# Kernel tuning notes

Hardware: AMD Instinct MI355X
Metric: run time of the kernel (lower is better)

## Reference

```python
import jax, jax.numpy as jnp
import numpy as np

N_SPIKES = 16384
N_UNITS = 256
N_NEIGHB = 128
RANK = 5
NC = 64
NC_OBS = 12
N_CAND = 10  # n_candidates*(n_search+1)+n_explore = 3*3+1
D = RANK * NC_OBS
LOG2PI = 1.8378770664093453


def setup_inputs() -> dict:
    key = jax.random.key(0)
    ks = jax.random.split(key, 8)
    features = jax.random.normal(ks[0], (N_SPIKES, RANK, NC_OBS), dtype=jnp.float32)
    mu = jax.random.normal(ks[1], (N_UNITS, RANK, NC), dtype=jnp.float32)
    # PSD inverse marginal covariances per neighborhood: A A^T / D + I
    A = jax.random.normal(ks[2], (N_NEIGHB, D, D), dtype=jnp.float32)
    Coo_inv = jnp.einsum('nij,nkj->nik', A, A) / D + jnp.eye(D, dtype=jnp.float32)
    # logdet of Coo = -logdet(Coo_inv)
    sign, ld = jnp.linalg.slogdet(Coo_inv)
    Coo_logdet = (-ld).astype(jnp.float32)
    log_proportions = jax.nn.log_softmax(jax.random.normal(ks[3], (N_UNITS,), dtype=jnp.float32))
    noise_log_prop = jnp.float32(-3.0)
    cands = jax.random.randint(ks[4], (N_SPIKES, N_CAND), 0, N_UNITS)
    nid = jax.random.randint(ks[5], (N_SPIKES,), 0, N_NEIGHB)
    # distinct observed channels per neighborhood, sorted
    perm = jnp.argsort(jax.random.uniform(ks[6], (N_NEIGHB, NC)), axis=1)
    obs_ix = jnp.sort(perm[:, :NC_OBS], axis=1)
    return {
        'features': features, 'mu': mu, 'Coo_inv': Coo_inv,
        'Coo_logdet': Coo_logdet, 'log_proportions': log_proportions,
        'noise_log_prop': noise_log_prop, 'cands': cands, 'nid': nid,
        'obs_ix': obs_ix,
    }


def reference(features, mu, Coo_inv, Coo_logdet, log_proportions, noise_log_prop, cands, nid, obs_ix):
    N, R, nco = features.shape
    Nu = mu.shape[0]
    C = cands.shape[1]
    Dd = R * nco
    # --- gather per-spike / per-candidate tables (load_batch) ---
    obs = obs_ix[nid]                                   # (N, nco)
    mu_c = mu[cands]                                    # (N, C, R, NC)
    nu = jnp.take_along_axis(mu_c, obs[:, None, None, :], axis=3)  # (N, C, R, nco)
    Cinv = Coo_inv[nid]                                 # (N, D, D)
    base = Coo_logdet[nid] + Dd * LOG2PI                # (N,)
    # --- truncated Gaussian log-likelihoods (te_batch) ---
    xf = features.reshape(N, Dd)
    xc = xf[:, None, :] - nu.reshape(N, C, Dd)          # (N, C, D)
    y = jnp.einsum('nde,nce->ncd', Cinv, xc)
    mahal = jnp.einsum('ncd,ncd->nc', y, xc)
    ll = log_proportions[cands] - 0.5 * (base[:, None] + mahal)
    yn = jnp.einsum('nde,ne->nd', Cinv, xf)
    mahal_noise = jnp.einsum('nd,nd->n', yn, xf)
    ll_noise = noise_log_prop - 0.5 * (base + mahal_noise)
    logliks = jnp.concatenate([ll, ll_noise[:, None]], axis=1)  # (N, C+1)
    Q = jax.nn.softmax(logliks, axis=1)
    # --- scatter-add sufficient statistics per unit ---
    Qc = Q[:, :C]
    seg = cands.reshape(-1)
    counts = jax.ops.segment_sum(Qc.reshape(-1), seg, num_segments=Nu)
    xw = (Qc[:, :, None] * xf[:, None, :]).reshape(N * C, Dd)
    xsum = jax.ops.segment_sum(xw, seg, num_segments=Nu)
    return jnp.concatenate([counts[:, None], xsum], axis=1)  # (Nu, D+1)
```

## Files before the change

### kernel.cpp

```cpp
#include <hip/hip_runtime.h>

#define N_SPIKES 16384
#define N_UNITS  256
#define N_NEIGHB 128
#define RANK     5
#define NC       64
#define NC_OBS   12
#define N_CAND   10
#define DD       60
#define DD4      15
#define OUT_COLS 61
#define OUT_SIZE (N_UNITS * OUT_COLS)
#define NSB      8
#define SCAP     192
#define CNT_PAD  4
#define CAP      (NSB * SCAP)
#define CPAD     64

__global__ __launch_bounds__(256) void precompute_kernel(
    const float* __restrict__ mu, const float* __restrict__ Coo_inv,
    const int* __restrict__ obs_ix, const float* __restrict__ log_prop,
    float* __restrict__ w_buf, float* __restrict__ b_buf,
    int* __restrict__ gcount)
{
    __shared__ float cinv[DD * CPAD];
    __shared__ float nu_lds[64 * 61];
    __shared__ float q2_lds[64 * 4];

    const int b   = blockIdx.x;
    const int h   = b >> 2;
    const int ub  = (b & 3) * 64;
    const int tid = threadIdx.x;

    if (tid < 16) gcount[b * 16 + tid] = 0;

    {
        const float* __restrict__ src = Coo_inv + h * DD * DD;
        for (int idx = tid; idx < DD * CPAD; idx += 256) {
            const int e = idx >> 6;
            const int c = idx & 63;
            cinv[idx] = (c < DD) ? src[e * DD + c] : 0.f;
        }
    }

    {
        const int ut  = tid >> 2;
        const int dqt = tid & 3;
        const float* __restrict__ mub = mu + (ub + ut) * (RANK * NC);
#pragma unroll
        for (int j = 0; j < DD4; ++j) {
            const int d  = dqt * DD4 + j;
            const int r  = d / NC_OBS;
            const int jj = d - r * NC_OBS;
            const int ch = obs_ix[h * NC_OBS + jj];
            nu_lds[ut * 61 + d] = mub[r * NC + ch];
        }
    }
    __syncthreads();

    const int lane = tid & 63;
    const int dq   = __builtin_amdgcn_readfirstlane(tid >> 6);
    const int u    = ub + lane;
    const int p    = h * N_UNITS + u;

    float wreg[16];
#pragma unroll
    for (int j = 0; j < 16; ++j) wreg[j] = 0.f;

    const float* __restrict__ Cslice = cinv + dq * 16;
#pragma unroll 4
    for (int e = 0; e < DD; ++e) {
        const float nu_e = nu_lds[lane * 61 + e];
        const float4* __restrict__ c4 =
            (const float4*)(Cslice + e * CPAD);
        const float4 c0 = c4[0], c1 = c4[1], c2 = c4[2], c3 = c4[3];
        wreg[ 0] = fmaf(c0.x, nu_e, wreg[ 0]);
        wreg[ 1] = fmaf(c0.y, nu_e, wreg[ 1]);
        wreg[ 2] = fmaf(c0.z, nu_e, wreg[ 2]);
        wreg[ 3] = fmaf(c0.w, nu_e, wreg[ 3]);
        wreg[ 4] = fmaf(c1.x, nu_e, wreg[ 4]);
        wreg[ 5] = fmaf(c1.y, nu_e, wreg[ 5]);
        wreg[ 6] = fmaf(c1.z, nu_e, wreg[ 6]);
        wreg[ 7] = fmaf(c1.w, nu_e, wreg[ 7]);
        wreg[ 8] = fmaf(c2.x, nu_e, wreg[ 8]);
        wreg[ 9] = fmaf(c2.y, nu_e, wreg[ 9]);
        wreg[10] = fmaf(c2.z, nu_e, wreg[10]);
        wreg[11] = fmaf(c2.w, nu_e, wreg[11]);
        wreg[12] = fmaf(c3.x, nu_e, wreg[12]);
        wreg[13] = fmaf(c3.y, nu_e, wreg[13]);
        wreg[14] = fmaf(c3.z, nu_e, wreg[14]);
        wreg[15] = fmaf(c3.w, nu_e, wreg[15]);
    }

    float q2 = 0.f;
#pragma unroll
    for (int j = 0; j < 16; ++j) {
        const int c = dq * 16 + j;
        const float nv = nu_lds[lane * 61 + (c < DD ? c : 0)];
        q2 += (c < DD) ? wreg[j] * nv : 0.f;
    }
    q2_lds[lane * 4 + dq] = q2;

    {
        float* __restrict__ wp = w_buf + p * DD + dq * 16;
#pragma unroll
        for (int k = 0; k < 4; ++k) {
            if (dq * 16 + k * 4 < DD) {
                float4 o;
                o.x = wreg[4*k+0]; o.y = wreg[4*k+1];
                o.z = wreg[4*k+2]; o.w = wreg[4*k+3];
                *(float4*)(wp + k * 4) = o;
            }
        }
    }

    __syncthreads();
    if (dq == 0) {
        const float q2s = q2_lds[lane * 4 + 0] + q2_lds[lane * 4 + 1]
                        + q2_lds[lane * 4 + 2] + q2_lds[lane * 4 + 3];
        b_buf[p] = log_prop[u] - 0.5f * q2s;
    }
}

__global__ __launch_bounds__(1024) void spike_bin_kernel(
    const float* __restrict__ features, const float* __restrict__ noise_lp,
    const int* __restrict__ cands, const int* __restrict__ nid,
    const float* __restrict__ w_buf, const float* __restrict__ b_buf,
    int* __restrict__ gcount, int2* __restrict__ bins)
{
    const int tid  = threadIdx.x;
    const int lane = tid & 63;
    const int wave = tid >> 6;
    const int c    = lane & 15;
    const int s    = lane >> 4;
    const int n    = blockIdx.x * 64 + wave * 4 + s;
    const int sb   = blockIdx.x & (NSB - 1);
    const bool act = (c < N_CAND);
    const int cc   = act ? c : (N_CAND - 1);

    const float4* __restrict__ f4 = (const float4*)features;
    const float4* __restrict__ w4 = (const float4*)w_buf;

    const int   h   = nid[n];
    const float nlp = noise_lp[0];
    const int   uc  = cands[n * N_CAND + cc];
    const int   p   = h * N_UNITS + uc;
    const float bb  = b_buf[p];

    float t = 0.f;
#pragma unroll
    for (int k = 0; k < DD4; ++k) {
        const float4 wv = w4[p * DD4 + k];
        const float4 xv = f4[n * DD4 + k];
        t += wv.x * xv.x + wv.y * xv.y + wv.z * xv.z + wv.w * xv.w;
    }
    float ll = act ? (bb + t) : -3.4e38f;

    float m = ll;
    m = fmaxf(m, __shfl_xor(m, 1, 16));
    m = fmaxf(m, __shfl_xor(m, 2, 16));
    m = fmaxf(m, __shfl_xor(m, 4, 16));
    m = fmaxf(m, __shfl_xor(m, 8, 16));
    m = fmaxf(m, nlp);
    const float e = act ? __expf(ll - m) : 0.f;
    float ssum = e;
    ssum += __shfl_xor(ssum, 1, 16);
    ssum += __shfl_xor(ssum, 2, 16);
    ssum += __shfl_xor(ssum, 4, 16);
    ssum += __shfl_xor(ssum, 8, 16);
    ssum += __expf(nlp - m);
    const float q = e / ssum;

    if (act && q > 0.f) {
        const int bi  = uc * NSB + sb;
        const int pos = atomicAdd(&gcount[bi * CNT_PAD], 1);
        if (pos < SCAP) bins[bi * SCAP + pos] = make_int2(n, __float_as_int(q));
    }
}

__global__ __launch_bounds__(512) void unit_accum_kernel(
    const float* __restrict__ features, const int* __restrict__ gcount,
    const int2* __restrict__ bins, float* __restrict__ out)
{
    __shared__ int2  rec[CAP];
    __shared__ float red[8][OUT_COLS];
    __shared__ int   cnts[NSB];
    __shared__ int   offs[NSB + 1];

    const int u    = blockIdx.x;
    const int tid  = threadIdx.x;
    const int lane = tid & 63;
    const int wave = tid >> 6;

    if (tid < NSB) {
        int c = gcount[(u * NSB + tid) * CNT_PAD];
        cnts[tid] = c < SCAP ? c : SCAP;
    }
    __syncthreads();
    if (tid == 0) {
        int o = 0;
#pragma unroll
        for (int sb = 0; sb < NSB; ++sb) { offs[sb] = o; o += cnts[sb]; }
        offs[NSB] = o;
    }
    __syncthreads();

    {
        const int base = offs[wave];
        const int cnt  = cnts[wave];
        const int2* __restrict__ src = bins + (u * NSB + wave) * SCAP;
        for (int i = lane; i < cnt; i += 64) rec[base + i] = src[i];
    }
    __syncthreads();

    const int total = offs[NSB];
    const int g = tid >> 4;
    const int l = lane & 15;

    const float4* __restrict__ f4 = (const float4*)features;
    float4 a = {0.f, 0.f, 0.f, 0.f};
    float sq = 0.f;

    for (int i = g; i < total; i += 32) {
        const int2 r = rec[i];
        const float q = __int_as_float(r.y);
        if (l < DD4) {
            const float4 xv = f4[r.x * DD4 + l];
            a.x = fmaf(q, xv.x, a.x);
            a.y = fmaf(q, xv.y, a.y);
            a.z = fmaf(q, xv.z, a.z);
            a.w = fmaf(q, xv.w, a.w);
        } else if (l == DD4) {
            sq += q;
        }
    }

    a.x += __shfl_xor(a.x, 16, 64);  a.x += __shfl_xor(a.x, 32, 64);
    a.y += __shfl_xor(a.y, 16, 64);  a.y += __shfl_xor(a.y, 32, 64);
    a.z += __shfl_xor(a.z, 16, 64);  a.z += __shfl_xor(a.z, 32, 64);
    a.w += __shfl_xor(a.w, 16, 64);  a.w += __shfl_xor(a.w, 32, 64);
    sq  += __shfl_xor(sq, 16, 64);   sq  += __shfl_xor(sq, 32, 64);

    if (lane < DD4) {
        red[wave][1 + 4*lane + 0] = a.x;
        red[wave][1 + 4*lane + 1] = a.y;
        red[wave][1 + 4*lane + 2] = a.z;
        red[wave][1 + 4*lane + 3] = a.w;
    } else if (lane == DD4) {
        red[wave][0] = sq;
    }
    __syncthreads();

    if (tid < OUT_COLS) {
        float ssum = 0.f;
#pragma unroll
        for (int w = 0; w < 8; ++w) ssum += red[w][tid];
        out[u * OUT_COLS + tid] = ssum;
    }
}

extern "C" void kernel_launch(void* const* d_in, const int* in_sizes, int n_in,
                              void* d_out, int out_size, void* d_ws, size_t ws_size,
                              hipStream_t stream) {
    const float* features    = (const float*)d_in[0];
    const float* mu          = (const float*)d_in[1];
    const float* Coo_inv     = (const float*)d_in[2];
    const float* log_prop    = (const float*)d_in[4];
    const float* noise_lp    = (const float*)d_in[5];
    const int*   cands       = (const int*)d_in[6];
    const int*   nid         = (const int*)d_in[7];
    const int*   obs_ix      = (const int*)d_in[8];
    float* out = (float*)d_out;

    char* ws = (char*)d_ws;
    float* w_buf  = (float*)ws;
    float* b_buf  = (float*)(ws + 7864320);
    int*   gcount = (int*)(ws + 7995392);
    int2*  bins   = (int2*)(ws + 8028160);

    precompute_kernel<<<512, 256, 0, stream>>>(mu, Coo_inv, obs_ix, log_prop,
                                               w_buf, b_buf, gcount);
    spike_bin_kernel<<<256, 1024, 0, stream>>>(features, noise_lp, cands, nid,
                                               w_buf, b_buf, gcount, bins);
    unit_accum_kernel<<<256, 512, 0, stream>>>(features, gcount, bins, out);
}
```

Before: 110.1 us.

## Pack bias into padded weight rows, batch loads, and unroll accumulation loop

Each weight row is padded to 64 floats and the bias is stored in the padding, so the spike kernel fetches weights and bias together in aligned float4 loads instead of a separate gather. The spike kernel preloads all weight and feature vectors into registers before the dot product, and runs 512-thread blocks across twice as many blocks. The accumulation kernel unrolls its record loop by four so more feature loads are in flight at once. The q>0 check before the atomic is dropped, and the register preloads may raise register pressure.

New measurement: 105.6 us. 1.04x faster.

```diff
diff --git a/kernel.cpp b/kernel.cpp
--- a/kernel.cpp
+++ b/kernel.cpp
@@ -9,6 +9,7 @@
 #define N_CAND   10
 #define DD       60
 #define DD4      15
+#define WROW4    16
 #define OUT_COLS 61
 #define OUT_SIZE (N_UNITS * OUT_COLS)
 #define NSB      8
@@ -20,8 +21,7 @@
 __global__ __launch_bounds__(256) void precompute_kernel(
     const float* __restrict__ mu, const float* __restrict__ Coo_inv,
     const int* __restrict__ obs_ix, const float* __restrict__ log_prop,
-    float* __restrict__ w_buf, float* __restrict__ b_buf,
-    int* __restrict__ gcount)
+    float* __restrict__ w_buf, int* __restrict__ gcount)
 {
     __shared__ float cinv[DD * CPAD];
     __shared__ float nu_lds[64 * 61];
@@ -102,7 +102,7 @@
     q2_lds[lane * 4 + dq] = q2;
 
     {
-        float* __restrict__ wp = w_buf + p * DD + dq * 16;
+        float* __restrict__ wp = w_buf + p * (WROW4 * 4) + dq * 16;
 #pragma unroll
         for (int k = 0; k < 4; ++k) {
             if (dq * 16 + k * 4 < DD) {
@@ -118,14 +118,16 @@
     if (dq == 0) {
         const float q2s = q2_lds[lane * 4 + 0] + q2_lds[lane * 4 + 1]
                         + q2_lds[lane * 4 + 2] + q2_lds[lane * 4 + 3];
-        b_buf[p] = log_prop[u] - 0.5f * q2s;
+        float4 bv;
+        bv.x = log_prop[u] - 0.5f * q2s; bv.y = 0.f; bv.z = 0.f; bv.w = 0.f;
+        *(float4*)(w_buf + p * (WROW4 * 4) + DD) = bv;
     }
 }
 
-__global__ __launch_bounds__(1024) void spike_bin_kernel(
+__global__ __launch_bounds__(512, 4) void spike_bin_kernel(
     const float* __restrict__ features, const float* __restrict__ noise_lp,
     const int* __restrict__ cands, const int* __restrict__ nid,
-    const float* __restrict__ w_buf, const float* __restrict__ b_buf,
+    const float* __restrict__ w_buf,
     int* __restrict__ gcount, int2* __restrict__ bins)
 {
     const int tid  = threadIdx.x;
@@ -133,7 +135,7 @@
     const int wave = tid >> 6;
     const int c    = lane & 15;
     const int s    = lane >> 4;
-    const int n    = blockIdx.x * 64 + wave * 4 + s;
+    const int n    = blockIdx.x * 32 + wave * 4 + s;
     const int sb   = blockIdx.x & (NSB - 1);
     const bool act = (c < N_CAND);
     const int cc   = act ? c : (N_CAND - 1);
@@ -145,15 +147,19 @@
     const float nlp = noise_lp[0];
     const int   uc  = cands[n * N_CAND + cc];
     const int   p   = h * N_UNITS + uc;
-    const float bb  = b_buf[p];
+
+    float4 wv[WROW4];
+#pragma unroll
+    for (int k = 0; k < WROW4; ++k) wv[k] = w4[p * WROW4 + k];
+    float4 xv[DD4];
+#pragma unroll
+    for (int k = 0; k < DD4; ++k) xv[k] = f4[n * DD4 + k];
 
     float t = 0.f;
 #pragma unroll
-    for (int k = 0; k < DD4; ++k) {
-        const float4 wv = w4[p * DD4 + k];
-        const float4 xv = f4[n * DD4 + k];
-        t += wv.x * xv.x + wv.y * xv.y + wv.z * xv.z + wv.w * xv.w;
-    }
+    for (int k = 0; k < DD4; ++k)
+        t += wv[k].x*xv[k].x + wv[k].y*xv[k].y + wv[k].z*xv[k].z + wv[k].w*xv[k].w;
+    const float bb = wv[DD4].x;
     float ll = act ? (bb + t) : -3.4e38f;
 
     float m = ll;
@@ -171,14 +177,14 @@
     ssum += __expf(nlp - m);
     const float q = e / ssum;
 
-    if (act && q > 0.f) {
+    if (act) {
         const int bi  = uc * NSB + sb;
         const int pos = atomicAdd(&gcount[bi * CNT_PAD], 1);
         if (pos < SCAP) bins[bi * SCAP + pos] = make_int2(n, __float_as_int(q));
     }
 }
 
-__global__ __launch_bounds__(512) void unit_accum_kernel(
+__global__ __launch_bounds__(512, 4) void unit_accum_kernel(
     const float* __restrict__ features, const int* __restrict__ gcount,
     const int2* __restrict__ bins, float* __restrict__ out)
 {
@@ -216,15 +222,42 @@
     const int total = offs[NSB];
     const int g = tid >> 4;
     const int l = lane & 15;
+    const bool dl = (l < DD4);
 
     const float4* __restrict__ f4 = (const float4*)features;
     float4 a = {0.f, 0.f, 0.f, 0.f};
     float sq = 0.f;
 
-    for (int i = g; i < total; i += 32) {
+    int i = g;
+    for (; i + 96 < total; i += 128) {
+        const int2 r0 = rec[i];
+        const int2 r1 = rec[i + 32];
+        const int2 r2 = rec[i + 64];
+        const int2 r3 = rec[i + 96];
+        const int li = dl ? l : 0;
+        const float4 x0 = f4[r0.x * DD4 + li];
+        const float4 x1 = f4[r1.x * DD4 + li];
+        const float4 x2 = f4[r2.x * DD4 + li];
+        const float4 x3 = f4[r3.x * DD4 + li];
+        const float q0 = __int_as_float(r0.y), q1 = __int_as_float(r1.y);
+        const float q2 = __int_as_float(r2.y), q3 = __int_as_float(r3.y);
+        if (dl) {
+            a.x = fmaf(q0, x0.x, a.x); a.y = fmaf(q0, x0.y, a.y);
+            a.z = fmaf(q0, x0.z, a.z); a.w = fmaf(q0, x0.w, a.w);
+            a.x = fmaf(q1, x1.x, a.x); a.y = fmaf(q1, x1.y, a.y);
+            a.z = fmaf(q1, x1.z, a.z); a.w = fmaf(q1, x1.w, a.w);
+            a.x = fmaf(q2, x2.x, a.x); a.y = fmaf(q2, x2.y, a.y);
+            a.z = fmaf(q2, x2.z, a.z); a.w = fmaf(q2, x2.w, a.w);
+            a.x = fmaf(q3, x3.x, a.x); a.y = fmaf(q3, x3.y, a.y);
+            a.z = fmaf(q3, x3.z, a.z); a.w = fmaf(q3, x3.w, a.w);
+        } else if (l == DD4) {
+            sq += q0 + q1 + q2 + q3;
+        }
+    }
+    for (; i < total; i += 32) {
         const int2 r = rec[i];
         const float q = __int_as_float(r.y);
-        if (l < DD4) {
+        if (dl) {
             const float4 xv = f4[r.x * DD4 + l];
             a.x = fmaf(q, xv.x, a.x);
             a.y = fmaf(q, xv.y, a.y);
@@ -274,13 +307,12 @@
 
     char* ws = (char*)d_ws;
     float* w_buf  = (float*)ws;
-    float* b_buf  = (float*)(ws + 7864320);
-    int*   gcount = (int*)(ws + 7995392);
-    int2*  bins   = (int2*)(ws + 8028160);
+    int*   gcount = (int*)(ws + 8388608);
+    int2*  bins   = (int2*)(ws + 8421376);
 
     precompute_kernel<<<512, 256, 0, stream>>>(mu, Coo_inv, obs_ix, log_prop,
-                                               w_buf, b_buf, gcount);
-    spike_bin_kernel<<<256, 1024, 0, stream>>>(features, noise_lp, cands, nid,
-                                               w_buf, b_buf, gcount, bins);
+                                               w_buf, gcount);
+    spike_bin_kernel<<<512, 512, 0, stream>>>(features, noise_lp, cands, nid,
+                                              w_buf, gcount, bins);
     unit_accum_kernel<<<256, 512, 0, stream>>>(features, gcount, bins, out);
 }
```
